# Kernel tuning notes

Measured on AMD Instinct MI355X. Metric: run time of the kernel, lower is better.

## Reference

```python
import jax, jax.numpy as jnp
import numpy as np

C, H, W = 3, 32, 32
DIM = C * H * W
NUM_CLUSTERS = 4096
BATCH = 8192


def setup_inputs() -> dict:
    key = jax.random.key(0)
    k_x, k_t, k_m = jax.random.split(key, 3)
    x = jax.random.normal(k_x, (BATCH, C, H, W), dtype=jnp.float32)
    t = jax.random.uniform(k_t, (1,), dtype=jnp.float32)
    means = jax.random.normal(k_m, (NUM_CLUSTERS, C, H, W), dtype=jnp.float32)
    # normalize each cluster mean to unit L2 norm over (C,H,W), as in __init__
    norms = jnp.sqrt(jnp.sum(means ** 2, axis=(1, 2, 3), keepdims=True))
    means = means / norms
    standard_dev = jnp.ones((1,), dtype=jnp.float32)  # sqrt(init_variance=1.0)
    return {"x": x, "t": t, "means": means, "standard_dev": standard_dev}


def reference(x, t, means, standard_dev):
    B = x.shape[0]
    x_f = x.reshape(B, -1)                      # [B, D]
    scale = jnp.exp(-t)                         # [1]
    variance = 1.0 - scale ** 2                 # [1]
    variance_t = scale ** 2 * standard_dev ** 2 + variance  # [1]

    sc = means.reshape(means.shape[0], -1) * scale          # [N, D] scaled clusters

    x_sq = jnp.sum(x_f ** 2, axis=-1, keepdims=True)        # [B, 1]
    c_sq = jnp.sum(sc ** 2, axis=-1)[None, :]               # [1, N]
    d2 = jnp.maximum(x_sq + c_sq - 2.0 * (x_f @ sc.T), 0.0)  # [B, N]

    weights = -0.5 * d2 / variance_t                        # [B, N]
    normalized_weights = jax.nn.softmax(weights, axis=-1)   # [B, N]

    cluster_term = normalized_weights @ sc                  # [B, D]

    denoiser_weight = scale ** 2 * standard_dev ** 2 / variance_t  # [1]
    out = denoiser_weight * x_f + (1.0 - denoiser_weight) * cluster_term
    out = out / scale
    return out.reshape(B, C, H, W)
```

## Files before the change

### kernel.cpp

```cpp
#include <hip/hip_runtime.h>
#include <hip/hip_bf16.h>
#include <math.h>
#include <stdint.h>

#define BATCH 8192
#define NCLUST 4096
#define DIM 3072

typedef __bf16 bf16;
typedef __bf16 bf16x4 __attribute__((ext_vector_type(4)));
typedef __bf16 bf16x8 __attribute__((ext_vector_type(8)));
typedef float f32x4 __attribute__((ext_vector_type(4)));
typedef int i32x4 __attribute__((ext_vector_type(4)));

__device__ __forceinline__ void get_scalars(const float* t, const float* sdv,
                                            float& scale, float& vt, float& dw) {
    float s = expf(-t[0]);
    float sd = sdv[0];
    float s2sd2 = s * s * sd * sd;
    float var = 1.0f - s * s;
    scale = s;
    vt = s2sd2 + var;
    dw = s2sd2 / vt;
}

__device__ __forceinline__ void async16(const bf16* g, bf16* l) {
    __builtin_amdgcn_global_load_lds(
        (const __attribute__((address_space(1))) void*)g,
        (__attribute__((address_space(3))) void*)l, 16, 0, 0);
}


__global__ __launch_bounds__(256) void cvt_x_kernel(const float* __restrict__ x,
                                                    bf16* __restrict__ xb, int n4) {
    int i = blockIdx.x * blockDim.x + threadIdx.x;
    if (i >= n4) return;
    float4 v = ((const float4*)x)[i];
    bf16x4 o = {(bf16)v.x, (bf16)v.y, (bf16)v.z, (bf16)v.w};
    ((bf16x4*)xb)[i] = o;
}

__global__ __launch_bounds__(256) void prep_sc_kernel(const float* __restrict__ means,
                                                      const float* __restrict__ t,
                                                      bf16* __restrict__ scb,
                                                      float* __restrict__ c_sq) {
    __shared__ float red[4];
    int row = blockIdx.x, tid = threadIdx.x;
    float scale = expf(-t[0]);
    const float4* m4 = (const float4*)(means + (size_t)row * DIM);
    bf16x4* o4 = (bf16x4*)(scb + (size_t)row * DIM);
    float s = 0.f;
#pragma unroll
    for (int j = 0; j < 3; ++j) {
        float4 v = m4[tid + 256 * j];
        float a = v.x * scale, b = v.y * scale, c = v.z * scale, d = v.w * scale;
        s += a * a + b * b + c * c + d * d;
        bf16x4 o = {(bf16)a, (bf16)b, (bf16)c, (bf16)d};
        o4[tid + 256 * j] = o;
    }
    for (int off = 32; off > 0; off >>= 1) s += __shfl_down(s, off);
    if ((tid & 63) == 0) red[tid >> 6] = s;
    __syncthreads();
    if (tid == 0) c_sq[row] = red[0] + red[1] + red[2] + red[3];
}

__global__ __launch_bounds__(256) void transpose_sc_kernel(const float* __restrict__ means,
                                                           const float* __restrict__ t,
                                                           bf16* __restrict__ scT) {
    __shared__ bf16 tile[64][65];
    float scale = expf(-t[0]);
    int tid = threadIdx.x;
    int tx = tid & 63, ty = tid >> 6;
    int d0 = blockIdx.x * 64, n0 = blockIdx.y * 64;
#pragma unroll
    for (int i = 0; i < 16; ++i) {
        int nr = ty + 4 * i;
        tile[nr][tx] = (bf16)(means[(size_t)(n0 + nr) * DIM + d0 + tx] * scale);
    }
    __syncthreads();
#pragma unroll
    for (int i = 0; i < 16; ++i) {
        int dr = ty + 4 * i;
        scT[(size_t)(d0 + dr) * NCLUST + n0 + tx] = tile[tx][dr];
    }
}


__device__ __forceinline__ void compute_tile(const bf16* asb, const bf16* bsb,
                                             f32x4 acc[4][4], int wr, int wc,
                                             int lrow, int swq) {
    bf16x8 av[4], bv[4];
#pragma unroll
    for (int ti = 0; ti < 4; ++ti)
        av[ti] = *(const bf16x8*)(asb + (wr * 64 + ti * 16 + lrow) * 32 + swq * 8);
#pragma unroll
    for (int tj = 0; tj < 4; ++tj)
        bv[tj] = *(const bf16x8*)(bsb + (wc * 64 + tj * 16 + lrow) * 32 + swq * 8);
#pragma unroll
    for (int ti = 0; ti < 4; ++ti)
#pragma unroll
        for (int tj = 0; tj < 4; ++tj)
            acc[ti][tj] = __builtin_amdgcn_mfma_f32_16x16x32_bf16(
                av[ti], bv[tj], acc[ti][tj], 0, 0, 0);
}

__global__ __launch_bounds__(256) void gemm_bt_kernel(
    const bf16* __restrict__ A, const bf16* __restrict__ B,
    int M, int N, int K, int lda,
    const float* __restrict__ t, const float* __restrict__ sdv,
    const float* __restrict__ c_sq, const float* __restrict__ xres,
    float* __restrict__ C, int epi) {
    __shared__ __attribute__((aligned(16))) bf16 As[2][128 * 32];
    __shared__ __attribute__((aligned(16))) bf16 Bs[2][128 * 32];

    const int tid = threadIdx.x;
    const int lane = tid & 63;
    const int w = tid >> 6;
    const int wr = w >> 1, wc = w & 1;
    const int lrow = lane & 15;
    const int lq = lane >> 4;
    const int swq = lq ^ ((lrow >> 1) & 3);
    const int m0 = blockIdx.y * 128, n0 = blockIdx.x * 128;

    const int c0 = tid;
    const int c1 = tid + 256;
    const int srow0 = c0 >> 2, skc0 = (c0 & 3) ^ ((srow0 >> 1) & 3);
    const int srow1 = c1 >> 2, skc1 = (c1 & 3) ^ ((srow1 >> 1) & 3);

    const bf16* gA0 = A + (size_t)(m0 + srow0) * lda + skc0 * 8;
    const bf16* gA1 = A + (size_t)(m0 + srow1) * lda + skc1 * 8;
    const bf16* gB0 = B + (size_t)(n0 + srow0) * K + skc0 * 8;
    const bf16* gB1 = B + (size_t)(n0 + srow1) * K + skc1 * 8;

    f32x4 acc[4][4];
#pragma unroll
    for (int i = 0; i < 4; ++i)
#pragma unroll
        for (int j = 0; j < 4; ++j) acc[i][j] = f32x4{0.f, 0.f, 0.f, 0.f};

    async16(gA0, &As[0][c0 * 8]);
    async16(gA1, &As[0][c1 * 8]);
    async16(gB0, &Bs[0][c0 * 8]);
    async16(gB1, &Bs[0][c1 * 8]);
    __syncthreads();

    const int nk = K >> 5;
    int buf = 0;
    for (int it = 0; it < nk - 1; ++it) {
        const int off = (it + 1) << 5;
        bf16* asn = &As[buf ^ 1][0];
        bf16* bsn = &Bs[buf ^ 1][0];
        async16(gA0 + off, asn + c0 * 8);
        async16(gA1 + off, asn + c1 * 8);
        async16(gB0 + off, bsn + c0 * 8);
        async16(gB1 + off, bsn + c1 * 8);

        compute_tile(&As[buf][0], &Bs[buf][0], acc, wr, wc, lrow, swq);

        __syncthreads();
        buf ^= 1;
    }
    compute_tile(&As[buf][0], &Bs[buf][0], acc, wr, wc, lrow, swq);

    float scale, vt, dw;
    get_scalars(t, sdv, scale, vt, dw);

    if (epi == 1) {
        const float inv_vt = 1.0f / vt;
#pragma unroll
        for (int ti = 0; ti < 4; ++ti) {
            int rbase = m0 + wr * 64 + ti * 16 + lq * 4;
#pragma unroll
            for (int tj = 0; tj < 4; ++tj) {
                int col = n0 + wc * 64 + tj * 16 + lrow;
                float csq = c_sq[col];
#pragma unroll
                for (int r = 0; r < 4; ++r)
                    __builtin_nontemporal_store(
                        (acc[ti][tj][r] - 0.5f * csq) * inv_vt,
                        &C[(size_t)(rbase + r) * N + col]);
            }
        }
    } else {
        const float inv_scale = 1.0f / scale;
        const float wx = dw * inv_scale;
        const float wcl = (1.0f - dw) * inv_scale;
#pragma unroll
        for (int ti = 0; ti < 4; ++ti) {
            int rbase = m0 + wr * 64 + ti * 16 + lq * 4;
#pragma unroll
            for (int tj = 0; tj < 4; ++tj) {
                int col = n0 + wc * 64 + tj * 16 + lrow;
#pragma unroll
                for (int r = 0; r < 4; ++r) {
                    size_t idx = (size_t)(rbase + r) * N + col;
                    float xv = __builtin_nontemporal_load(&xres[idx]);
                    __builtin_nontemporal_store(wx * xv + wcl * acc[ti][tj][r],
                                                &C[idx]);
                }
            }
        }
    }
}

__global__ __launch_bounds__(256) void softmax_kernel(float* __restrict__ S) {
    __shared__ float red[4];
    int b = blockIdx.x, tid = threadIdx.x;
    int lane = tid & 63;
    float* srow = S + (size_t)b * NCLUST;
    const f32x4* s4 = (const f32x4*)srow;
    f32x4 v[4];
#pragma unroll
    for (int j = 0; j < 4; ++j) v[j] = __builtin_nontemporal_load(&s4[tid + 256 * j]);

    float mx = -3.4e38f;
#pragma unroll
    for (int j = 0; j < 4; ++j)
        mx = fmaxf(mx, fmaxf(fmaxf(v[j][0], v[j][1]), fmaxf(v[j][2], v[j][3])));
    for (int off = 32; off > 0; off >>= 1) mx = fmaxf(mx, __shfl_down(mx, off));
    if (lane == 0) red[tid >> 6] = mx;
    __syncthreads();
    mx = fmaxf(fmaxf(red[0], red[1]), fmaxf(red[2], red[3]));
    __syncthreads();

    float e[16];
    float s = 0.f;
#pragma unroll
    for (int j = 0; j < 4; ++j) {
#pragma unroll
        for (int q = 0; q < 4; ++q) {
            e[4 * j + q] = expf(v[j][q] - mx);
            s += e[4 * j + q];
        }
    }
    for (int off = 32; off > 0; off >>= 1) s += __shfl_down(s, off);
    if (lane == 0) red[tid >> 6] = s;
    __syncthreads();
    s = red[0] + red[1] + red[2] + red[3];
    float inv = 1.0f / s;

    bf16x4* p4 = (bf16x4*)srow;
#pragma unroll
    for (int j = 0; j < 4; ++j) {
        bf16x4 o = {(bf16)(e[4 * j + 0] * inv), (bf16)(e[4 * j + 1] * inv),
                    (bf16)(e[4 * j + 2] * inv), (bf16)(e[4 * j + 3] * inv)};
        p4[tid + 256 * j] = o;
    }
}

extern "C" void kernel_launch(void* const* d_in, const int* in_sizes, int n_in,
                              void* d_out, int out_size, void* d_ws, size_t ws_size,
                              hipStream_t stream) {
    const float* x = (const float*)d_in[0];
    const float* t = (const float*)d_in[1];
    const float* means = (const float*)d_in[2];
    const float* sdv = (const float*)d_in[3];
    float* out = (float*)d_out;

    char* ws = (char*)d_ws;
    bf16* xb = (bf16*)ws;
    bf16* scb = (bf16*)(ws + 50331648);
    bf16* scT = (bf16*)(ws + 75497472);
    float* c_sq = (float*)(ws + 100663296);
    float* S = (float*)(ws + 100679680);

    cvt_x_kernel<<<(BATCH * DIM / 4 + 255) / 256, 256, 0, stream>>>(x, xb, BATCH * DIM / 4);
    prep_sc_kernel<<<NCLUST, 256, 0, stream>>>(means, t, scb, c_sq);
    transpose_sc_kernel<<<dim3(DIM / 64, NCLUST / 64), 256, 0, stream>>>(means, t, scT);

    gemm_bt_kernel<<<dim3(NCLUST / 128, BATCH / 128), 256, 0, stream>>>(
        xb, scb, BATCH, NCLUST, DIM, DIM, t, sdv, c_sq, nullptr, S, 1);

    softmax_kernel<<<BATCH, 256, 0, stream>>>(S);

    gemm_bt_kernel<<<dim3(DIM / 128, BATCH / 128), 256, 0, stream>>>(
        (const bf16*)S, scT, BATCH, DIM, NCLUST, 2 * NCLUST, t, sdv, nullptr, x, out, 2);
}
```

Before: 865.2 us.

## Replace 128x128 GEMM with 256x256 eight-wave pipelined MFMA kernel

Both GEMMs now use a 256x256 tile with 512 threads, BK=64, and a four-phase schedule. Each half-tile of A and B is reloaded asynchronously into LDS while MFMAs run on the other half, with explicit vmcnt/lgkmcnt waits, barriers and s_setprio raising. The larger tile gives more reuse per byte loaded and hides global-load latency, with an 8-way XOR swizzle to avoid LDS bank conflicts. In exchange it uses more LDS and registers per block (128 accumulator floats per lane) and leaves fewer blocks for the second GEMM, so occupancy and tail effects are a risk.

```diff
diff --git a/kernel.cpp b/kernel.cpp
--- a/kernel.cpp
+++ b/kernel.cpp
@@ -11,7 +11,6 @@
 typedef __bf16 bf16x4 __attribute__((ext_vector_type(4)));
 typedef __bf16 bf16x8 __attribute__((ext_vector_type(8)));
 typedef float f32x4 __attribute__((ext_vector_type(4)));
-typedef int i32x4 __attribute__((ext_vector_type(4)));
 
 __device__ __forceinline__ void get_scalars(const float* t, const float* sdv,
                                             float& scale, float& vt, float& dw) {
@@ -86,81 +85,151 @@
 }
 
 
-__device__ __forceinline__ void compute_tile(const bf16* asb, const bf16* bsb,
-                                             f32x4 acc[4][4], int wr, int wc,
-                                             int lrow, int swq) {
-    bf16x8 av[4], bv[4];
-#pragma unroll
-    for (int ti = 0; ti < 4; ++ti)
-        av[ti] = *(const bf16x8*)(asb + (wr * 64 + ti * 16 + lrow) * 32 + swq * 8);
-#pragma unroll
-    for (int tj = 0; tj < 4; ++tj)
-        bv[tj] = *(const bf16x8*)(bsb + (wc * 64 + tj * 16 + lrow) * 32 + swq * 8);
-#pragma unroll
-    for (int ti = 0; ti < 4; ++ti)
-#pragma unroll
-        for (int tj = 0; tj < 4; ++tj)
-            acc[ti][tj] = __builtin_amdgcn_mfma_f32_16x16x32_bf16(
-                av[ti], bv[tj], acc[ti][tj], 0, 0, 0);
-}
-
-__global__ __launch_bounds__(256) void gemm_bt_kernel(
+__device__ __forceinline__ void stage2(const bf16* g, size_t ld64, bf16* lds,
+                                       int koff, int tid) {
+    async16(g + koff, lds + tid * 8);
+    async16(g + koff + ld64, lds + (tid + 512) * 8);
+}
+
+__global__ __launch_bounds__(512, 2) void gemm256_kernel(
     const bf16* __restrict__ A, const bf16* __restrict__ B,
     int M, int N, int K, int lda,
     const float* __restrict__ t, const float* __restrict__ sdv,
     const float* __restrict__ c_sq, const float* __restrict__ xres,
     float* __restrict__ C, int epi) {
-    __shared__ __attribute__((aligned(16))) bf16 As[2][128 * 32];
-    __shared__ __attribute__((aligned(16))) bf16 Bs[2][128 * 32];
+    __shared__ __attribute__((aligned(16))) bf16 As[2][2][128 * 64];
+    __shared__ __attribute__((aligned(16))) bf16 Bs[2][2][128 * 64];
 
     const int tid = threadIdx.x;
     const int lane = tid & 63;
-    const int w = tid >> 6;
-    const int wr = w >> 1, wc = w & 1;
+    const int wid = tid >> 6;
+    const int wr = wid >> 2;
+    const int wc = wid & 3;
     const int lrow = lane & 15;
     const int lq = lane >> 4;
-    const int swq = lq ^ ((lrow >> 1) & 3);
-    const int m0 = blockIdx.y * 128, n0 = blockIdx.x * 128;
-
-    const int c0 = tid;
-    const int c1 = tid + 256;
-    const int srow0 = c0 >> 2, skc0 = (c0 & 3) ^ ((srow0 >> 1) & 3);
-    const int srow1 = c1 >> 2, skc1 = (c1 & 3) ^ ((srow1 >> 1) & 3);
-
-    const bf16* gA0 = A + (size_t)(m0 + srow0) * lda + skc0 * 8;
-    const bf16* gA1 = A + (size_t)(m0 + srow1) * lda + skc1 * 8;
-    const bf16* gB0 = B + (size_t)(n0 + srow0) * K + skc0 * 8;
-    const bf16* gB1 = B + (size_t)(n0 + srow1) * K + skc1 * 8;
-
-    f32x4 acc[4][4];
-#pragma unroll
-    for (int i = 0; i < 4; ++i)
+    const int m0 = blockIdx.y * 256, n0 = blockIdx.x * 256;
+
+    const int srow = tid >> 3;
+    const int sgc = (tid & 7) ^ (srow & 7);
+    const bf16* gA0 = A + (size_t)(m0 + srow) * lda + sgc * 8;
+    const bf16* gA1 = gA0 + (size_t)128 * lda;
+    const bf16* gB0 = B + (size_t)(n0 + srow) * K + sgc * 8;
+    const bf16* gB1 = gB0 + (size_t)128 * K;
+    const size_t a64 = (size_t)64 * lda;
+    const size_t b64 = (size_t)64 * K;
+
+    const int x7 = lrow & 7;
+    const int pos0 = lq ^ x7;
+    const int pos1 = (4 + lq) ^ x7;
+    const int aoff0 = lrow * 64 + pos0 * 8;
+    const int aoff1 = lrow * 64 + pos1 * 8;
+    const int brbase = (wc & 1) * 64 + lrow;
+    const int boff0 = brbase * 64 + pos0 * 8;
+    const int boff1 = brbase * 64 + pos1 * 8;
+
+    f32x4 acc[8][4];
+#pragma unroll
+    for (int i = 0; i < 8; ++i)
 #pragma unroll
         for (int j = 0; j < 4; ++j) acc[i][j] = f32x4{0.f, 0.f, 0.f, 0.f};
 
-    async16(gA0, &As[0][c0 * 8]);
-    async16(gA1, &As[0][c1 * 8]);
-    async16(gB0, &Bs[0][c0 * 8]);
-    async16(gB1, &Bs[0][c1 * 8]);
-    __syncthreads();
-
-    const int nk = K >> 5;
-    int buf = 0;
-    for (int it = 0; it < nk - 1; ++it) {
-        const int off = (it + 1) << 5;
-        bf16* asn = &As[buf ^ 1][0];
-        bf16* bsn = &Bs[buf ^ 1][0];
-        async16(gA0 + off, asn + c0 * 8);
-        async16(gA1 + off, asn + c1 * 8);
-        async16(gB0 + off, bsn + c0 * 8);
-        async16(gB1 + off, bsn + c1 * 8);
-
-        compute_tile(&As[buf][0], &Bs[buf][0], acc, wr, wc, lrow, swq);
-
-        __syncthreads();
-        buf ^= 1;
-    }
-    compute_tile(&As[buf][0], &Bs[buf][0], acc, wr, wc, lrow, swq);
+    const int NT = K >> 6;
+
+    stage2(gA0, a64, &As[0][0][0], 0, tid);
+    stage2(gA1, a64, &As[0][1][0], 0, tid);
+    stage2(gB0, b64, &Bs[0][0][0], 0, tid);
+    stage2(gB1, b64, &Bs[0][1][0], 0, tid);
+    stage2(gB0, b64, &Bs[1][0][0], 64, tid);
+    stage2(gA0, a64, &As[1][0][0], 64, tid);
+    asm volatile("s_waitcnt vmcnt(4)" ::: "memory");
+    __builtin_amdgcn_s_barrier();
+
+    for (int tt = 0; tt < NT; ++tt) {
+        const int buf = tt & 1;
+        const bf16* Aw = &As[buf][wr][0];
+        const bf16* Bw = &Bs[buf][wc >> 1][0];
+        bf16x8 a_[4][2], bA[2][2], bB[2][2];
+
+#pragma unroll
+        for (int i = 0; i < 4; ++i) {
+            a_[i][0] = *(const bf16x8*)(Aw + i * 1024 + aoff0);
+            a_[i][1] = *(const bf16x8*)(Aw + i * 1024 + aoff1);
+        }
+#pragma unroll
+        for (int j = 0; j < 2; ++j) {
+            bA[j][0] = *(const bf16x8*)(Bw + j * 1024 + boff0);
+            bA[j][1] = *(const bf16x8*)(Bw + j * 1024 + boff1);
+        }
+        if (tt + 1 < NT) stage2(gB1, b64, &Bs[buf ^ 1][1][0], (tt + 1) << 6, tid);
+        __builtin_amdgcn_s_barrier();
+        asm volatile("s_waitcnt lgkmcnt(0)" ::: "memory");
+        __builtin_amdgcn_s_setprio(1);
+#pragma unroll
+        for (int i = 0; i < 4; ++i)
+#pragma unroll
+            for (int j = 0; j < 2; ++j) {
+                acc[i][j] = __builtin_amdgcn_mfma_f32_16x16x32_bf16(a_[i][0], bA[j][0], acc[i][j], 0, 0, 0);
+                acc[i][j] = __builtin_amdgcn_mfma_f32_16x16x32_bf16(a_[i][1], bA[j][1], acc[i][j], 0, 0, 0);
+            }
+        __builtin_amdgcn_s_setprio(0);
+        __builtin_amdgcn_s_barrier();
+
+#pragma unroll
+        for (int j = 0; j < 2; ++j) {
+            bB[j][0] = *(const bf16x8*)(Bw + (2 + j) * 1024 + boff0);
+            bB[j][1] = *(const bf16x8*)(Bw + (2 + j) * 1024 + boff1);
+        }
+        if (tt + 1 < NT) stage2(gA1, a64, &As[buf ^ 1][1][0], (tt + 1) << 6, tid);
+        __builtin_amdgcn_s_barrier();
+        asm volatile("s_waitcnt lgkmcnt(0)" ::: "memory");
+        __builtin_amdgcn_s_setprio(1);
+#pragma unroll
+        for (int i = 0; i < 4; ++i)
+#pragma unroll
+            for (int j = 0; j < 2; ++j) {
+                acc[i][2 + j] = __builtin_amdgcn_mfma_f32_16x16x32_bf16(a_[i][0], bB[j][0], acc[i][2 + j], 0, 0, 0);
+                acc[i][2 + j] = __builtin_amdgcn_mfma_f32_16x16x32_bf16(a_[i][1], bB[j][1], acc[i][2 + j], 0, 0, 0);
+            }
+        __builtin_amdgcn_s_setprio(0);
+        __builtin_amdgcn_s_barrier();
+
+#pragma unroll
+        for (int i = 0; i < 4; ++i) {
+            a_[i][0] = *(const bf16x8*)(Aw + (4 + i) * 1024 + aoff0);
+            a_[i][1] = *(const bf16x8*)(Aw + (4 + i) * 1024 + aoff1);
+        }
+        if (tt + 2 < NT) stage2(gB0, b64, &Bs[buf][0][0], (tt + 2) << 6, tid);
+        __builtin_amdgcn_s_barrier();
+        asm volatile("s_waitcnt lgkmcnt(0)" ::: "memory");
+        __builtin_amdgcn_s_setprio(1);
+#pragma unroll
+        for (int i = 0; i < 4; ++i)
+#pragma unroll
+            for (int j = 0; j < 2; ++j) {
+                acc[4 + i][2 + j] = __builtin_amdgcn_mfma_f32_16x16x32_bf16(a_[i][0], bB[j][0], acc[4 + i][2 + j], 0, 0, 0);
+                acc[4 + i][2 + j] = __builtin_amdgcn_mfma_f32_16x16x32_bf16(a_[i][1], bB[j][1], acc[4 + i][2 + j], 0, 0, 0);
+            }
+        __builtin_amdgcn_s_setprio(0);
+        __builtin_amdgcn_s_barrier();
+
+        if (tt + 2 < NT) stage2(gA0, a64, &As[buf][0][0], (tt + 2) << 6, tid);
+        __builtin_amdgcn_s_barrier();
+        __builtin_amdgcn_s_setprio(1);
+#pragma unroll
+        for (int i = 0; i < 4; ++i)
+#pragma unroll
+            for (int j = 0; j < 2; ++j) {
+                acc[4 + i][j] = __builtin_amdgcn_mfma_f32_16x16x32_bf16(a_[i][0], bA[j][0], acc[4 + i][j], 0, 0, 0);
+                acc[4 + i][j] = __builtin_amdgcn_mfma_f32_16x16x32_bf16(a_[i][1], bA[j][1], acc[4 + i][j], 0, 0, 0);
+            }
+        __builtin_amdgcn_s_setprio(0);
+        if (tt < NT - 2) {
+            asm volatile("s_waitcnt vmcnt(4)" ::: "memory");
+        } else if (tt == NT - 2) {
+            asm volatile("s_waitcnt vmcnt(0)" ::: "memory");
+        }
+        __builtin_amdgcn_s_barrier();
+    }
 
     float scale, vt, dw;
     get_scalars(t, sdv, scale, vt, dw);
@@ -168,16 +237,16 @@
     if (epi == 1) {
         const float inv_vt = 1.0f / vt;
 #pragma unroll
-        for (int ti = 0; ti < 4; ++ti) {
-            int rbase = m0 + wr * 64 + ti * 16 + lq * 4;
-#pragma unroll
-            for (int tj = 0; tj < 4; ++tj) {
-                int col = n0 + wc * 64 + tj * 16 + lrow;
+        for (int m = 0; m < 8; ++m) {
+            int rbase = m0 + wr * 128 + m * 16 + lq * 4;
+#pragma unroll
+            for (int n = 0; n < 4; ++n) {
+                int col = n0 + wc * 64 + n * 16 + lrow;
                 float csq = c_sq[col];
 #pragma unroll
                 for (int r = 0; r < 4; ++r)
                     __builtin_nontemporal_store(
-                        (acc[ti][tj][r] - 0.5f * csq) * inv_vt,
+                        (acc[m][n][r] - 0.5f * csq) * inv_vt,
                         &C[(size_t)(rbase + r) * N + col]);
             }
         }
@@ -186,16 +255,16 @@
         const float wx = dw * inv_scale;
         const float wcl = (1.0f - dw) * inv_scale;
 #pragma unroll
-        for (int ti = 0; ti < 4; ++ti) {
-            int rbase = m0 + wr * 64 + ti * 16 + lq * 4;
-#pragma unroll
-            for (int tj = 0; tj < 4; ++tj) {
-                int col = n0 + wc * 64 + tj * 16 + lrow;
+        for (int m = 0; m < 8; ++m) {
+            int rbase = m0 + wr * 128 + m * 16 + lq * 4;
+#pragma unroll
+            for (int n = 0; n < 4; ++n) {
+                int col = n0 + wc * 64 + n * 16 + lrow;
 #pragma unroll
                 for (int r = 0; r < 4; ++r) {
                     size_t idx = (size_t)(rbase + r) * N + col;
                     float xv = __builtin_nontemporal_load(&xres[idx]);
-                    __builtin_nontemporal_store(wx * xv + wcl * acc[ti][tj][r],
+                    __builtin_nontemporal_store(wx * xv + wcl * acc[m][n][r],
                                                 &C[idx]);
                 }
             }
@@ -268,11 +337,11 @@
     prep_sc_kernel<<<NCLUST, 256, 0, stream>>>(means, t, scb, c_sq);
     transpose_sc_kernel<<<dim3(DIM / 64, NCLUST / 64), 256, 0, stream>>>(means, t, scT);
 
-    gemm_bt_kernel<<<dim3(NCLUST / 128, BATCH / 128), 256, 0, stream>>>(
+    gemm256_kernel<<<dim3(NCLUST / 256, BATCH / 256), 512, 0, stream>>>(
         xb, scb, BATCH, NCLUST, DIM, DIM, t, sdv, c_sq, nullptr, S, 1);
 
     softmax_kernel<<<BATCH, 256, 0, stream>>>(S);
 
-    gemm_bt_kernel<<<dim3(DIM / 128, BATCH / 128), 256, 0, stream>>>(
+    gemm256_kernel<<<dim3(DIM / 256, BATCH / 256), 512, 0, stream>>>(
         (const bf16*)S, scT, BATCH, DIM, NCLUST, 2 * NCLUST, t, sdv, nullptr, x, out, 2);
 }
```

Result: faster. 707.4 us (-18.2%).
